# Performance work log

Measured on AMD Instinct MI355X. Metric: run time of the kernel, lower is better.

Reference implementation:

```python
import jax, jax.numpy as jnp
import numpy as np

N, E, DIN, H, DOUT, NBLK = 50000, 300000, 963, 256, 3, 6


def gconv(x, src, dst, ew, W, Wl, b):
    # support = x @ W ; out[i] = sum_j ew_ij * support[j] + x[i] @ W_loop + b
    sup = x @ W
    agg = jax.ops.segment_sum(ew[:, None] * sup[src], dst, num_segments=N)
    return agg + x @ Wl + b


def setup_inputs() -> dict:
    key = jax.random.key(0)
    ks = jax.random.split(key, 16)
    s = 0.05
    x = jax.random.normal(ks[0], (N, DIN), jnp.float32)
    src = jax.random.randint(ks[1], (E,), 0, N, dtype=jnp.int32)
    dst = jax.random.randint(ks[2], (E,), 0, N, dtype=jnp.int32)
    ew = jax.random.uniform(ks[3], (E,), jnp.float32)
    W1 = jax.random.normal(ks[4], (DIN, H), jnp.float32) * s
    Wl1 = jax.random.normal(ks[5], (DIN, H), jnp.float32) * s
    b1 = jnp.zeros((H,), jnp.float32)
    # stacked residual-block weights: [NBLK, 2 convs, H, H]
    blkW = jax.random.normal(ks[6], (NBLK, 2, H, H), jnp.float32) * s
    blkWl = jax.random.normal(ks[7], (NBLK, 2, H, H), jnp.float32) * s
    blkb = jnp.zeros((NBLK, 2, H), jnp.float32)
    W2 = jax.random.normal(ks[8], (H, DOUT), jnp.float32) * s
    Wl2 = jax.random.normal(ks[9], (H, DOUT), jnp.float32) * s
    b2 = jnp.zeros((DOUT,), jnp.float32)
    return dict(x=x, src=src, dst=dst, ew=ew, W1=W1, Wl1=Wl1, b1=b1,
                blkW=blkW, blkWl=blkWl, blkb=blkb, W2=W2, Wl2=Wl2, b2=b2)


def reference(x, src, dst, ew, W1, Wl1, b1, blkW, blkWl, blkb, W2, Wl2, b2):
    h = jax.nn.relu(gconv(x, src, dst, ew, W1, Wl1, b1))

    def block(h, p):
        W, Wl, b = p  # W: [2,H,H]
        y = jax.nn.relu(gconv(h, src, dst, ew, W[0], Wl[0], b[0]))
        y = jax.nn.relu(gconv(y, src, dst, ew, W[1], Wl[1], b[1]))
        return (h + y) * 0.5, None

    x_hidden, _ = jax.lax.scan(block, h, (blkW, blkWl, blkb))
    x_out = gconv(x_hidden, src, dst, ew, W2, Wl2, b2)
    return (x_out, x_hidden)
```

## Files before the change

kernel.cpp:

```cpp
#include <hip/hip_runtime.h>

typedef __attribute__((ext_vector_type(8))) short short8;
typedef __attribute__((ext_vector_type(4))) float f32x4;
typedef __attribute__((ext_vector_type(4), aligned(4))) float f32x4u;

constexpr int kN = 50000;
constexpr int kE = 300000;
constexpr int kDIN = 963;
constexpr int kH = 256;
constexpr int kNBLK = 6;

__device__ inline unsigned short f2bf(float f) {
    unsigned u = __float_as_uint(f);
    u = u + 0x7FFFu + ((u >> 16) & 1u);
    return (unsigned short)(u >> 16);
}
__device__ inline float bf2f(unsigned short s) {
    return __uint_as_float(((unsigned)s) << 16);
}

__device__ inline void gload_lds16(const void* g, void* l) {
    __builtin_amdgcn_global_load_lds(
        (const __attribute__((address_space(1))) void*)g,
        (__attribute__((address_space(3))) void*)l, 16, 0, 0);
}

__global__ __launch_bounds__(512) void gemm_l1(
    const float* __restrict__ Av, const unsigned short* __restrict__ Bt,
    const float* __restrict__ bias,
    unsigned short* __restrict__ supb, unsigned short* __restrict__ tpreb,
    int M, int Kpad, int Kvalid, int Astride)
{
    __shared__ __align__(16) char smem[81920];
    char* As  = smem;
    char* Bs0 = smem + 16384;
    char* Bs1 = smem + 49152;

    const int tid = threadIdx.x;
    const int wid = tid >> 6;
    const int lane = tid & 63;
    const int wr = wid >> 2, wc = wid & 3;

    const int nwg = gridDim.x;
    const int q = nwg >> 3, r = nwg & 7;
    const int xcd = blockIdx.x & 7, idx = blockIdx.x >> 3;
    const int t = (xcd < r ? xcd * (q + 1) : r * (q + 1) + (xcd - r) * q) + idx;
    const int r0 = t * 128;

    f32x4 acc[2][4][4];
#pragma unroll
    for (int hf = 0; hf < 2; ++hf)
#pragma unroll
        for (int i = 0; i < 4; ++i)
#pragma unroll
            for (int j = 0; j < 4; ++j) acc[hf][i][j] = f32x4{0.f, 0.f, 0.f, 0.f};

    const int l_row = lane >> 3;
    const int l_c   = lane & 7;

    for (int k0 = 0; k0 < Kpad; k0 += 64) {
#pragma unroll
        for (int p = 0; p < 4; ++p) {
            int row = wid * 32 + p * 8 + l_row;
            int csw = l_c ^ (row & 7);
            const unsigned short* g0 = Bt + (long)row * Kpad + k0 + csw * 8;
            gload_lds16(g0, Bs0 + (wid * 32 + p * 8) * 128);
            const unsigned short* g1 = Bt + (long)(256 + row) * Kpad + k0 + csw * 8;
            gload_lds16(g1, Bs1 + (wid * 32 + p * 8) * 128);
        }
        {
            const int row = tid >> 2;
            const int kq = tid & 3;
            int grow = r0 + row; if (grow >= M) grow = M - 1;
            const float* ar = Av + (long)grow * Astride;
#pragma unroll
            for (int j = 0; j < 2; ++j) {
                int k16 = kq * 2 + j;
                int kb = k0 + k16 * 8;
                short8 v;
                if (kb + 8 <= Kvalid) {
                    f32x4u f0 = *(const f32x4u*)(ar + kb);
                    f32x4u f1 = *(const f32x4u*)(ar + kb + 4);
#pragma unroll
                    for (int ii = 0; ii < 4; ++ii) {
                        v[ii]     = (short)f2bf(f0[ii]);
                        v[ii + 4] = (short)f2bf(f1[ii]);
                    }
                } else {
#pragma unroll
                    for (int ii = 0; ii < 8; ++ii) {
                        int k = kb + ii;
                        float f = (k < Kvalid) ? ar[k] : 0.f;
                        v[ii] = (short)f2bf(f);
                    }
                }
                *(short8*)(As + row * 128 + ((k16 ^ (row & 7)) << 4)) = v;
            }
        }
        __syncthreads();
#pragma unroll
        for (int kk = 0; kk < 2; ++kk) {
            const int kg = kk * 4 + (lane >> 4);
            short8 af[4];
#pragma unroll
            for (int nr = 0; nr < 4; ++nr) {
                int row = wr * 64 + nr * 16 + (lane & 15);
                af[nr] = *(const short8*)(As + row * 128 + ((kg ^ (row & 7)) << 4));
            }
#pragma unroll
            for (int hf = 0; hf < 2; ++hf) {
                const char* Bs = hf ? Bs1 : Bs0;
                short8 bfr[4];
#pragma unroll
                for (int mc = 0; mc < 4; ++mc) {
                    int row = wc * 64 + mc * 16 + (lane & 15);
                    bfr[mc] = *(const short8*)(Bs + row * 128 + ((kg ^ (row & 7)) << 4));
                }
#pragma unroll
                for (int mc = 0; mc < 4; ++mc)
#pragma unroll
                    for (int nr = 0; nr < 4; ++nr)
                        acc[hf][mc][nr] = __builtin_amdgcn_mfma_f32_16x16x32_bf16(
                            bfr[mc], af[nr], acc[hf][mc][nr], 0, 0, 0);
            }
        }
        __syncthreads();
    }

    float* eL = (float*)smem;
    const int wrow = wr * 16 + (lane & 15);
    const int qc = (lane >> 4) << 2;

#pragma unroll
    for (int hf = 0; hf < 2; ++hf) {
        unsigned short* outp = hf ? tpreb : supb;
        for (int nr = 0; nr < 4; ++nr) {
            __syncthreads();
#pragma unroll
            for (int mc = 0; mc < 4; ++mc) {
                const int col = wc * 64 + mc * 16 + qc;
                f32x4 v = acc[hf][mc][nr];
                if (hf) v += *(const f32x4*)(bias + col);
                const int c16 = col >> 2;
                *(f32x4*)(eL + wrow * 256 + ((c16 ^ wrow) << 2)) = v;
            }
            __syncthreads();
            const int tr = tid >> 4, j = tid & 15;
            const int gr = r0 + (tr >> 4) * 64 + nr * 16 + (tr & 15);
            if (gr < M) {
#pragma unroll
                for (int p = 0; p < 2; ++p) {
                    const int u = j + 16 * p;
                    f32x4 lo = *(const f32x4*)(eL + tr * 256 + (((2 * u) ^ tr) << 2));
                    f32x4 hi = *(const f32x4*)(eL + tr * 256 + (((2 * u + 1) ^ tr) << 2));
                    uint4 pk;
                    pk.x = (unsigned)f2bf(lo[0]) | ((unsigned)f2bf(lo[1]) << 16);
                    pk.y = (unsigned)f2bf(lo[2]) | ((unsigned)f2bf(lo[3]) << 16);
                    pk.z = (unsigned)f2bf(hi[0]) | ((unsigned)f2bf(hi[1]) << 16);
                    pk.w = (unsigned)f2bf(hi[2]) | ((unsigned)f2bf(hi[3]) << 16);
                    *(uint4*)(outp + (long)gr * 256 + u * 8) = pk;
                }
            }
        }
    }
}

template<int RES>
__global__ __launch_bounds__(256) void gemm_blk(
    const unsigned short* __restrict__ act, const unsigned short* __restrict__ xagg,
    const unsigned short* __restrict__ Bt, const float* __restrict__ bias,
    const unsigned short* __restrict__ hbf_res,
    unsigned short* __restrict__ outbf, float* __restrict__ hf32)
{
    __shared__ __align__(16) char smem[32768];
    char* As = smem;
    char* Bs = smem + 16384;

    const int tid = threadIdx.x;
    const int wid = tid >> 6;
    const int lane = tid & 63;
    const int wr = wid >> 1, wc = wid & 1;

    const int nwg = gridDim.x;
    const int q = nwg >> 3, r = nwg & 7;
    const int xcd = blockIdx.x & 7, idx = blockIdx.x >> 3;
    const int t = (xcd < r ? xcd * (q + 1) : r * (q + 1) + (xcd - r) * q) + idx;
    const int r0 = (t >> 1) * 128;
    const int c0 = (t & 1) * 128;

    f32x4 acc[4][4];
#pragma unroll
    for (int i = 0; i < 4; ++i)
#pragma unroll
        for (int j = 0; j < 4; ++j) acc[i][j] = f32x4{0.f, 0.f, 0.f, 0.f};

    const int l_row = lane >> 3;
    const int l_c   = lane & 7;

    for (int k0 = 0; k0 < 512; k0 += 64) {
#pragma unroll
        for (int p = 0; p < 4; ++p) {
            int row = wid * 32 + p * 8 + l_row;
            int csw = l_c ^ (row & 7);
            const unsigned short* g = Bt + (long)(c0 + row) * 512 + k0 + csw * 8;
            gload_lds16(g, Bs + (wid * 32 + p * 8) * 128);
        }
        const unsigned short* Asrc = (k0 < 256) ? (act + k0) : (xagg + (k0 - 256));
#pragma unroll
        for (int p = 0; p < 4; ++p) {
            int row = wid * 32 + p * 8 + l_row;
            int grow = r0 + row; if (grow >= kN) grow = kN - 1;
            int csw = l_c ^ (row & 7);
            const unsigned short* g = Asrc + (long)grow * 256 + csw * 8;
            gload_lds16(g, As + (wid * 32 + p * 8) * 128);
        }
        __syncthreads();
#pragma unroll
        for (int kk = 0; kk < 2; ++kk) {
            short8 af[4], bfr[4];
            const int kg = kk * 4 + (lane >> 4);
#pragma unroll
            for (int nr = 0; nr < 4; ++nr) {
                int row = wr * 64 + nr * 16 + (lane & 15);
                af[nr] = *(const short8*)(As + row * 128 + ((kg ^ (row & 7)) << 4));
            }
#pragma unroll
            for (int mc = 0; mc < 4; ++mc) {
                int row = wc * 64 + mc * 16 + (lane & 15);
                bfr[mc] = *(const short8*)(Bs + row * 128 + ((kg ^ (row & 7)) << 4));
            }
#pragma unroll
            for (int mc = 0; mc < 4; ++mc)
#pragma unroll
                for (int nr = 0; nr < 4; ++nr)
                    acc[mc][nr] = __builtin_amdgcn_mfma_f32_16x16x32_bf16(
                        bfr[mc], af[nr], acc[mc][nr], 0, 0, 0);
        }
        __syncthreads();
    }

    float* eL = (float*)smem;
    const int wrow = wr * 16 + (lane & 15);
    const int qc = (lane >> 4) << 2;

    for (int nr = 0; nr < 4; ++nr) {
        __syncthreads();
#pragma unroll
        for (int mc = 0; mc < 4; ++mc) {
            const int col = wc * 64 + mc * 16 + qc;
            f32x4 v = acc[mc][nr] + *(const f32x4*)(bias + c0 + col);
            const int c16 = col >> 2;
            *(f32x4*)(eL + wrow * 128 + ((c16 ^ wrow) << 2)) = v;
        }
        __syncthreads();
        const int tr = tid >> 3, j = tid & 7;
        const int gr = r0 + (tr >> 4) * 64 + nr * 16 + (tr & 15);
        if (gr < kN) {
#pragma unroll
            for (int p = 0; p < 2; ++p) {
                const int u = j + 8 * p;
                f32x4 lo = *(const f32x4*)(eL + tr * 128 + (((2 * u) ^ tr) << 2));
                f32x4 hi = *(const f32x4*)(eL + tr * 128 + (((2 * u + 1) ^ tr) << 2));
#pragma unroll
                for (int ii = 0; ii < 4; ++ii) {
                    lo[ii] = fmaxf(lo[ii], 0.f);
                    hi[ii] = fmaxf(hi[ii], 0.f);
                }
                const long gcol = (long)gr * 256 + c0 + u * 8;
                if (RES >= 1) {
                    uint4 hv = *(const uint4*)(hbf_res + gcol);
                    lo[0] = (bf2f((unsigned short)(hv.x & 0xFFFF)) + lo[0]) * 0.5f;
                    lo[1] = (bf2f((unsigned short)(hv.x >> 16))    + lo[1]) * 0.5f;
                    lo[2] = (bf2f((unsigned short)(hv.y & 0xFFFF)) + lo[2]) * 0.5f;
                    lo[3] = (bf2f((unsigned short)(hv.y >> 16))    + lo[3]) * 0.5f;
                    hi[0] = (bf2f((unsigned short)(hv.z & 0xFFFF)) + hi[0]) * 0.5f;
                    hi[1] = (bf2f((unsigned short)(hv.z >> 16))    + hi[1]) * 0.5f;
                    hi[2] = (bf2f((unsigned short)(hv.w & 0xFFFF)) + hi[2]) * 0.5f;
                    hi[3] = (bf2f((unsigned short)(hv.w >> 16))    + hi[3]) * 0.5f;
                }
                if (RES == 2) {
                    *(f32x4*)(hf32 + gcol)     = lo;
                    *(f32x4*)(hf32 + gcol + 4) = hi;
                }
                uint4 pk;
                pk.x = (unsigned)f2bf(lo[0]) | ((unsigned)f2bf(lo[1]) << 16);
                pk.y = (unsigned)f2bf(lo[2]) | ((unsigned)f2bf(lo[3]) << 16);
                pk.z = (unsigned)f2bf(hi[0]) | ((unsigned)f2bf(hi[1]) << 16);
                pk.w = (unsigned)f2bf(hi[2]) | ((unsigned)f2bf(hi[3]) << 16);
                *(uint4*)(outbf + gcol) = pk;
            }
        }
    }
}

template<int MODE>
__global__ __launch_bounds__(256) void agg16_kernel(
    const unsigned short* __restrict__ srcbuf, const unsigned short* __restrict__ tpreb,
    const int* __restrict__ rowptr, const int* __restrict__ e_src,
    const float* __restrict__ e_w, unsigned short* __restrict__ outb)
{
    const int tid = threadIdx.x;
    const int sub = tid >> 5;
    const int l   = tid & 31;
    const long node = (long)blockIdx.x * 8 + sub;
    if (node >= kN) return;
    const int c0 = l * 8;

    f32x4 a0 = {0.f, 0.f, 0.f, 0.f}, a1 = {0.f, 0.f, 0.f, 0.f};
    if (MODE == 1) {
        uint4 tv = *(const uint4*)(tpreb + node * 256 + c0);
        a0[0] = bf2f((unsigned short)(tv.x & 0xFFFF)); a0[1] = bf2f((unsigned short)(tv.x >> 16));
        a0[2] = bf2f((unsigned short)(tv.y & 0xFFFF)); a0[3] = bf2f((unsigned short)(tv.y >> 16));
        a1[0] = bf2f((unsigned short)(tv.z & 0xFFFF)); a1[1] = bf2f((unsigned short)(tv.z >> 16));
        a1[2] = bf2f((unsigned short)(tv.w & 0xFFFF)); a1[3] = bf2f((unsigned short)(tv.w >> 16));
    }

    int b = rowptr[node];
    const int e = rowptr[node + 1];

#define ACC16(V, W) \
    a0[0] += (W) * bf2f((unsigned short)((V).x & 0xFFFF)); \
    a0[1] += (W) * bf2f((unsigned short)((V).x >> 16));    \
    a0[2] += (W) * bf2f((unsigned short)((V).y & 0xFFFF)); \
    a0[3] += (W) * bf2f((unsigned short)((V).y >> 16));    \
    a1[0] += (W) * bf2f((unsigned short)((V).z & 0xFFFF)); \
    a1[1] += (W) * bf2f((unsigned short)((V).z >> 16));    \
    a1[2] += (W) * bf2f((unsigned short)((V).w & 0xFFFF)); \
    a1[3] += (W) * bf2f((unsigned short)((V).w >> 16));

    for (; b + 4 <= e; b += 4) {
        const int s0 = e_src[b],     s1 = e_src[b + 1];
        const int s2 = e_src[b + 2], s3 = e_src[b + 3];
        const float w0 = e_w[b],     w1 = e_w[b + 1];
        const float w2 = e_w[b + 2], w3 = e_w[b + 3];
        uint4 v0 = *(const uint4*)(srcbuf + (long)s0 * 256 + c0);
        uint4 v1 = *(const uint4*)(srcbuf + (long)s1 * 256 + c0);
        uint4 v2 = *(const uint4*)(srcbuf + (long)s2 * 256 + c0);
        uint4 v3 = *(const uint4*)(srcbuf + (long)s3 * 256 + c0);
        ACC16(v0, w0) ACC16(v1, w1) ACC16(v2, w2) ACC16(v3, w3)
    }
    for (; b < e; ++b) {
        const int s = e_src[b];
        const float w = e_w[b];
        uint4 v = *(const uint4*)(srcbuf + (long)s * 256 + c0);
        ACC16(v, w)
    }
#undef ACC16

    if (MODE == 1) {
#pragma unroll
        for (int ii = 0; ii < 4; ++ii) {
            a0[ii] = fmaxf(a0[ii], 0.f);
            a1[ii] = fmaxf(a1[ii], 0.f);
        }
    }
    uint4 pk;
    pk.x = (unsigned)f2bf(a0[0]) | ((unsigned)f2bf(a0[1]) << 16);
    pk.y = (unsigned)f2bf(a0[2]) | ((unsigned)f2bf(a0[3]) << 16);
    pk.z = (unsigned)f2bf(a1[0]) | ((unsigned)f2bf(a1[1]) << 16);
    pk.w = (unsigned)f2bf(a1[2]) | ((unsigned)f2bf(a1[3]) << 16);
    *(uint4*)(outb + node * 256 + c0) = pk;
}

__global__ __launch_bounds__(256) void cvt_w1_kernel(
    const float* __restrict__ W1, const float* __restrict__ Wl1,
    unsigned short* __restrict__ out)
{
    int idx = blockIdx.x * 256 + threadIdx.x;
    if (idx >= 512 * 1024) return;
    int c = idx >> 10, k = idx & 1023;
    float v = 0.f;
    if (k < kDIN) v = (c < 256) ? W1[(long)k * 256 + c] : Wl1[(long)k * 256 + (c - 256)];
    out[idx] = f2bf(v);
}

__global__ __launch_bounds__(256) void cvt_blk_kernel(
    const float* __restrict__ blkW, const float* __restrict__ blkWl,
    unsigned short* __restrict__ out)
{
    int idx = blockIdx.x * 256 + threadIdx.x;
    if (idx >= 12 * 256 * 512) return;
    int l = idx >> 17;
    int rem = idx & 131071;
    int c = rem >> 9, k = rem & 511;
    float v = (k < 256) ? blkWl[((long)l * 256 + k) * 256 + c]
                        : blkW[((long)l * 256 + (k - 256)) * 256 + c];
    out[idx] = f2bf(v);
}

__global__ __launch_bounds__(256) void hist_kernel(const int* __restrict__ dst,
                                                   int* __restrict__ counts)
{
    int e = blockIdx.x * 256 + threadIdx.x;
    if (e < kE) atomicAdd(&counts[dst[e]], 1);
}

__global__ __launch_bounds__(1024) void scan1_kernel(
    const int* __restrict__ counts, int* __restrict__ rowptr, int* __restrict__ bsum)
{
    __shared__ int s[1024];
    const int tid = threadIdx.x;
    const int g = blockIdx.x * 1024 + tid;
    const int v = (g < kN) ? counts[g] : 0;
    s[tid] = v; __syncthreads();
    for (int off = 1; off < 1024; off <<= 1) {
        int tv = (tid >= off) ? s[tid - off] : 0;
        __syncthreads();
        s[tid] += tv;
        __syncthreads();
    }
    if (g < kN) rowptr[g] = s[tid] - v;
    if (tid == 1023) bsum[blockIdx.x] = s[1023];
}

__global__ __launch_bounds__(64) void scan2_kernel(int* __restrict__ bsum, int nb)
{
    __shared__ int s[64];
    const int tid = threadIdx.x;
    const int v = (tid < nb) ? bsum[tid] : 0;
    s[tid] = v; __syncthreads();
    for (int off = 1; off < 64; off <<= 1) {
        int tv = (tid >= off) ? s[tid - off] : 0;
        __syncthreads();
        s[tid] += tv;
        __syncthreads();
    }
    if (tid < nb) bsum[tid] = s[tid] - v;
}

__global__ __launch_bounds__(256) void scan3_kernel(
    int* __restrict__ rowptr, const int* __restrict__ bsum, int* __restrict__ cursor)
{
    int g = blockIdx.x * 256 + threadIdx.x;
    if (g < kN) {
        int r = rowptr[g] + bsum[g >> 10];
        rowptr[g] = r;
        cursor[g] = r;
    }
    if (g == 0) rowptr[kN] = kE;
}

__global__ __launch_bounds__(256) void fill_kernel(
    const int* __restrict__ src, const int* __restrict__ dst,
    const float* __restrict__ ew, int* __restrict__ cursor,
    int* __restrict__ e_src, float* __restrict__ e_w)
{
    int e = blockIdx.x * 256 + threadIdx.x;
    if (e >= kE) return;
    int d = dst[e];
    int pos = atomicAdd(&cursor[d], 1);
    e_src[pos] = src[e];
    e_w[pos] = ew[e];
}

__global__ __launch_bounds__(64) void final_layer_kernel(
    const unsigned short* __restrict__ hbf, const float* __restrict__ W2,
    const float* __restrict__ Wl2, const float* __restrict__ b2,
    float* __restrict__ sup2, float* __restrict__ x_out)
{
    const int row = blockIdx.x;
    const int lane = threadIdx.x;
    const unsigned short* hr = hbf + (long)row * kH;
    float accW[3] = {0.f, 0.f, 0.f};
    float accL[3] = {0.f, 0.f, 0.f};
#pragma unroll
    for (int kb = 0; kb < kH / 64; ++kb) {
        int k = kb * 64 + lane;
        float v = bf2f(hr[k]);
#pragma unroll
        for (int c = 0; c < 3; ++c) {
            accW[c] = fmaf(v, W2[k * 3 + c], accW[c]);
            accL[c] = fmaf(v, Wl2[k * 3 + c], accL[c]);
        }
    }
#pragma unroll
    for (int off = 32; off > 0; off >>= 1) {
#pragma unroll
        for (int c = 0; c < 3; ++c) {
            accW[c] += __shfl_down(accW[c], off);
            accL[c] += __shfl_down(accL[c], off);
        }
    }
    if (lane == 0) {
#pragma unroll
        for (int c = 0; c < 3; ++c) {
            sup2[row * 3 + c] = accW[c];
            x_out[row * 3 + c] = accL[c] + b2[c];
        }
    }
}

__global__ __launch_bounds__(256) void scatter3_kernel(
    const float* __restrict__ sup2, const int* __restrict__ src,
    const int* __restrict__ dst, const float* __restrict__ ew,
    float* __restrict__ x_out)
{
    int e = blockIdx.x * 256 + threadIdx.x;
    if (e >= kE) return;
    int s = src[e];
    int d = dst[e];
    float w = ew[e];
#pragma unroll
    for (int c = 0; c < 3; ++c)
        atomicAdd(&x_out[(long)d * 3 + c], w * sup2[(long)s * 3 + c]);
}

extern "C" void kernel_launch(void* const* d_in, const int* in_sizes, int n_in,
                              void* d_out, int out_size, void* d_ws, size_t ws_size,
                              hipStream_t stream)
{
    const float* x    = (const float*)d_in[0];
    const int*   src  = (const int*)d_in[1];
    const int*   dst  = (const int*)d_in[2];
    const float* ew   = (const float*)d_in[3];
    const float* W1   = (const float*)d_in[4];
    const float* Wl1  = (const float*)d_in[5];
    const float* b1   = (const float*)d_in[6];
    const float* blkW  = (const float*)d_in[7];
    const float* blkWl = (const float*)d_in[8];
    const float* blkb  = (const float*)d_in[9];
    const float* W2   = (const float*)d_in[10];
    const float* Wl2  = (const float*)d_in[11];
    const float* b2   = (const float*)d_in[12];

    float* out   = (float*)d_out;
    float* x_out = out;
    float* h     = out + (long)kN * 3;

    char* w = (char*)d_ws;
    size_t off = 0;
    auto carve = [&](size_t bytes) { char* p = w + off; off = (off + bytes + 255) & ~(size_t)255; return p; };
    unsigned short* supb  = (unsigned short*)carve(12800000UL * 2);
    unsigned short* tpreb = (unsigned short*)carve(12800000UL * 2);
    unsigned short* tact  = (unsigned short*)carve(12800000UL * 2);
    unsigned short* hbf   = (unsigned short*)carve(12800000UL * 2);
    unsigned short* w1c   = (unsigned short*)carve(512UL * 1024 * 2);
    unsigned short* blkc  = (unsigned short*)carve(12UL * 256 * 512 * 2);
    int*   e_src  = (int*)carve(kE * 4);
    float* e_w    = (float*)carve(kE * 4);
    int*   counts = (int*)carve(50176 * 4);
    int*   rowptr = (int*)carve(50176 * 4);
    int*   cursor = (int*)carve(50176 * 4);
    int*   bsum   = (int*)carve(64 * 4);
    float* sup2   = (float*)carve((long)kN * 3 * 4);
    unsigned short* xagg = tpreb;

    hipMemsetAsync(counts, 0, 50176 * 4, stream);
    hist_kernel<<<(kE + 255) / 256, 256, 0, stream>>>(dst, counts);
    scan1_kernel<<<49, 1024, 0, stream>>>(counts, rowptr, bsum);
    scan2_kernel<<<1, 64, 0, stream>>>(bsum, 49);
    scan3_kernel<<<(kN + 255) / 256, 256, 0, stream>>>(rowptr, bsum, cursor);
    fill_kernel<<<(kE + 255) / 256, 256, 0, stream>>>(src, dst, ew, cursor, e_src, e_w);

    cvt_w1_kernel<<<2048, 256, 0, stream>>>(W1, Wl1, w1c);
    cvt_blk_kernel<<<6144, 256, 0, stream>>>(blkW, blkWl, blkc);

    const int l1_grid  = (kN + 127) / 128;
    const int blk_grid = 2 * ((kN + 127) / 128);
    const int agg_grid = (kN + 7) / 8;

    gemm_l1<<<l1_grid, 512, 0, stream>>>(x, w1c, b1, supb, tpreb,
                                         kN, 1024, kDIN, kDIN);
    agg16_kernel<1><<<agg_grid, 256, 0, stream>>>(supb, tpreb, rowptr, e_src, e_w, hbf);

    for (int l = 0; l < 2 * kNBLK; ++l) {
        const unsigned short* act_in = (l & 1) ? tact : hbf;
        unsigned short* act_out      = (l & 1) ? hbf : tact;
        agg16_kernel<0><<<agg_grid, 256, 0, stream>>>(act_in, nullptr, rowptr, e_src, e_w, xagg);
        const unsigned short* B = blkc + (long)l * 256 * 512;
        const float* bb = blkb + (long)l * 256;
        if (l & 1) {
            if (l == 2 * kNBLK - 1)
                gemm_blk<2><<<blk_grid, 256, 0, stream>>>(act_in, xagg, B, bb, hbf, act_out, h);
            else
                gemm_blk<1><<<blk_grid, 256, 0, stream>>>(act_in, xagg, B, bb, hbf, act_out, nullptr);
        } else {
            gemm_blk<0><<<blk_grid, 256, 0, stream>>>(act_in, xagg, B, bb, nullptr, act_out, nullptr);
        }
    }

    final_layer_kernel<<<kN, 64, 0, stream>>>(hbf, W2, Wl2, b2, sup2, x_out);
    scatter3_kernel<<<(kE + 255) / 256, 256, 0, stream>>>(sup2, src, dst, ew, x_out);
}
```

Before: 955.1 us.

## Pre-convert x to padded bf16 and split layer-1 GEMM by output half; widen aggregation per lane

Adds a pass that converts x to a zero-padded bf16 buffer, then runs a new layer-1 GEMM that streams A and B straight into LDS with async global-to-LDS loads. The grid is split so each workgroup computes either the support or the self-loop half, using an XCD-aware tile mapping. This avoids converting fp32 to bf16 inside the GEMM mainloop, at the cost of an extra ~100MB write and read pass and of reading the A tile twice. The aggregation kernel now uses 16 lanes per node with 32-byte loads per lane, doubling the work per lane and halving the number of threads.

```diff
diff --git a/kernel.cpp b/kernel.cpp
--- a/kernel.cpp
+++ b/kernel.cpp
@@ -23,6 +23,138 @@
     __builtin_amdgcn_global_load_lds(
         (const __attribute__((address_space(1))) void*)g,
         (__attribute__((address_space(3))) void*)l, 16, 0, 0);
+}
+
+__global__ __launch_bounds__(128) void xcvt_kernel(
+    const float* __restrict__ x, unsigned short* __restrict__ xbf)
+{
+    const int row = blockIdx.x;
+    const int kb = threadIdx.x * 8;
+    const float* xr = x + (long)row * kDIN;
+    short8 v;
+    if (kb + 8 <= kDIN) {
+        f32x4u f0 = *(const f32x4u*)(xr + kb);
+        f32x4u f1 = *(const f32x4u*)(xr + kb + 4);
+#pragma unroll
+        for (int ii = 0; ii < 4; ++ii) {
+            v[ii]     = (short)f2bf(f0[ii]);
+            v[ii + 4] = (short)f2bf(f1[ii]);
+        }
+    } else {
+#pragma unroll
+        for (int ii = 0; ii < 8; ++ii) {
+            int k = kb + ii;
+            v[ii] = (short)((k < kDIN) ? f2bf(xr[k]) : 0);
+        }
+    }
+    *(short8*)(xbf + (long)row * 1024 + kb) = v;
+}
+
+__global__ __launch_bounds__(512) void gemm_l1_bf(
+    const unsigned short* __restrict__ xbf, const unsigned short* __restrict__ Bt,
+    const float* __restrict__ bias,
+    unsigned short* __restrict__ supb, unsigned short* __restrict__ tpreb)
+{
+    __shared__ __align__(16) char smem[49152];
+    char* As = smem;
+    char* Bs = smem + 16384;
+
+    const int tid = threadIdx.x;
+    const int wid = tid >> 6;
+    const int lane = tid & 63;
+    const int wr = wid >> 2, wc = wid & 3;
+
+    const int nwg = gridDim.x;
+    const int q = nwg >> 3, r = nwg & 7;
+    const int xcd = blockIdx.x & 7, idx = blockIdx.x >> 3;
+    const int t = (xcd < r ? xcd * (q + 1) : r * (q + 1) + (xcd - r) * q) + idx;
+    const int r0 = (t >> 1) * 128;
+    const int c0 = (t & 1) * 256;
+
+    f32x4 acc[4][4];
+#pragma unroll
+    for (int i = 0; i < 4; ++i)
+#pragma unroll
+        for (int j = 0; j < 4; ++j) acc[i][j] = f32x4{0.f, 0.f, 0.f, 0.f};
+
+    const int l_row = lane >> 3;
+    const int l_c   = lane & 7;
+
+    for (int k0 = 0; k0 < 1024; k0 += 64) {
+#pragma unroll
+        for (int p = 0; p < 4; ++p) {
+            int row = wid * 32 + p * 8 + l_row;
+            int csw = l_c ^ (row & 7);
+            const unsigned short* g = Bt + (long)(c0 + row) * 1024 + k0 + csw * 8;
+            gload_lds16(g, Bs + (wid * 32 + p * 8) * 128);
+        }
+#pragma unroll
+        for (int p = 0; p < 2; ++p) {
+            int row = wid * 16 + p * 8 + l_row;
+            int grow = r0 + row; if (grow >= kN) grow = kN - 1;
+            int csw = l_c ^ (row & 7);
+            const unsigned short* g = xbf + (long)grow * 1024 + k0 + csw * 8;
+            gload_lds16(g, As + (wid * 16 + p * 8) * 128);
+        }
+        __syncthreads();
+#pragma unroll
+        for (int kk = 0; kk < 2; ++kk) {
+            short8 af[4], bfr[4];
+            const int kg = kk * 4 + (lane >> 4);
+#pragma unroll
+            for (int nr = 0; nr < 4; ++nr) {
+                int row = wr * 64 + nr * 16 + (lane & 15);
+                af[nr] = *(const short8*)(As + row * 128 + ((kg ^ (row & 7)) << 4));
+            }
+#pragma unroll
+            for (int mc = 0; mc < 4; ++mc) {
+                int row = wc * 64 + mc * 16 + (lane & 15);
+                bfr[mc] = *(const short8*)(Bs + row * 128 + ((kg ^ (row & 7)) << 4));
+            }
+#pragma unroll
+            for (int mc = 0; mc < 4; ++mc)
+#pragma unroll
+                for (int nr = 0; nr < 4; ++nr)
+                    acc[mc][nr] = __builtin_amdgcn_mfma_f32_16x16x32_bf16(
+                        bfr[mc], af[nr], acc[mc][nr], 0, 0, 0);
+        }
+        __syncthreads();
+    }
+
+    const bool isSup = (c0 == 0);
+    unsigned short* outp = isSup ? supb : tpreb;
+    float* eL = (float*)smem;
+    const int wrow = wr * 16 + (lane & 15);
+    const int qc = (lane >> 4) << 2;
+
+    for (int nr = 0; nr < 4; ++nr) {
+        __syncthreads();
+#pragma unroll
+        for (int mc = 0; mc < 4; ++mc) {
+            const int col = wc * 64 + mc * 16 + qc;
+            f32x4 v = acc[mc][nr];
+            if (!isSup) v += *(const f32x4*)(bias + col);
+            const int c16 = col >> 2;
+            *(f32x4*)(eL + wrow * 256 + ((c16 ^ wrow) << 2)) = v;
+        }
+        __syncthreads();
+        const int tr = tid >> 4, j = tid & 15;
+        const int gr = r0 + (tr >> 4) * 64 + nr * 16 + (tr & 15);
+        if (gr < kN) {
+#pragma unroll
+            for (int p = 0; p < 2; ++p) {
+                const int u = j + 16 * p;
+                f32x4 lo = *(const f32x4*)(eL + tr * 256 + (((2 * u) ^ tr) << 2));
+                f32x4 hi = *(const f32x4*)(eL + tr * 256 + (((2 * u + 1) ^ tr) << 2));
+                uint4 pk;
+                pk.x = (unsigned)f2bf(lo[0]) | ((unsigned)f2bf(lo[1]) << 16);
+                pk.y = (unsigned)f2bf(lo[2]) | ((unsigned)f2bf(lo[3]) << 16);
+                pk.z = (unsigned)f2bf(hi[0]) | ((unsigned)f2bf(hi[1]) << 16);
+                pk.w = (unsigned)f2bf(hi[2]) | ((unsigned)f2bf(hi[3]) << 16);
+                *(uint4*)(outp + (long)gr * 256 + u * 8) = pk;
+            }
+        }
+    }
 }
 
 __global__ __launch_bounds__(512) void gemm_l1(
@@ -147,7 +279,7 @@
             __syncthreads();
             const int tr = tid >> 4, j = tid & 15;
             const int gr = r0 + (tr >> 4) * 64 + nr * 16 + (tr & 15);
-            if (gr < M) {
+            if (gr < kN) {
 #pragma unroll
                 for (int p = 0; p < 2; ++p) {
                     const int u = j + 16 * p;
@@ -300,66 +432,81 @@
     const float* __restrict__ e_w, unsigned short* __restrict__ outb)
 {
     const int tid = threadIdx.x;
-    const int sub = tid >> 5;
-    const int l   = tid & 31;
-    const long node = (long)blockIdx.x * 8 + sub;
+    const int sub = tid >> 4;
+    const int l   = tid & 15;
+    const long node = (long)blockIdx.x * 16 + sub;
     if (node >= kN) return;
-    const int c0 = l * 8;
-
-    f32x4 a0 = {0.f, 0.f, 0.f, 0.f}, a1 = {0.f, 0.f, 0.f, 0.f};
+    const int c0 = l * 16;
+
+    f32x4 a0 = {0.f,0.f,0.f,0.f}, a1 = {0.f,0.f,0.f,0.f};
+    f32x4 a2 = {0.f,0.f,0.f,0.f}, a3 = {0.f,0.f,0.f,0.f};
+
+#define UNPK(A0, A1, V, W) \
+    A0[0] += (W) * bf2f((unsigned short)((V).x & 0xFFFF)); \
+    A0[1] += (W) * bf2f((unsigned short)((V).x >> 16));    \
+    A0[2] += (W) * bf2f((unsigned short)((V).y & 0xFFFF)); \
+    A0[3] += (W) * bf2f((unsigned short)((V).y >> 16));    \
+    A1[0] += (W) * bf2f((unsigned short)((V).z & 0xFFFF)); \
+    A1[1] += (W) * bf2f((unsigned short)((V).z >> 16));    \
+    A1[2] += (W) * bf2f((unsigned short)((V).w & 0xFFFF)); \
+    A1[3] += (W) * bf2f((unsigned short)((V).w >> 16));
+
     if (MODE == 1) {
-        uint4 tv = *(const uint4*)(tpreb + node * 256 + c0);
-        a0[0] = bf2f((unsigned short)(tv.x & 0xFFFF)); a0[1] = bf2f((unsigned short)(tv.x >> 16));
-        a0[2] = bf2f((unsigned short)(tv.y & 0xFFFF)); a0[3] = bf2f((unsigned short)(tv.y >> 16));
-        a1[0] = bf2f((unsigned short)(tv.z & 0xFFFF)); a1[1] = bf2f((unsigned short)(tv.z >> 16));
-        a1[2] = bf2f((unsigned short)(tv.w & 0xFFFF)); a1[3] = bf2f((unsigned short)(tv.w >> 16));
+        uint4 t0 = *(const uint4*)(tpreb + node * 256 + c0);
+        uint4 t1 = *(const uint4*)(tpreb + node * 256 + c0 + 8);
+        UNPK(a0, a1, t0, 1.f)
+        UNPK(a2, a3, t1, 1.f)
     }
 
     int b = rowptr[node];
     const int e = rowptr[node + 1];
-
-#define ACC16(V, W) \
-    a0[0] += (W) * bf2f((unsigned short)((V).x & 0xFFFF)); \
-    a0[1] += (W) * bf2f((unsigned short)((V).x >> 16));    \
-    a0[2] += (W) * bf2f((unsigned short)((V).y & 0xFFFF)); \
-    a0[3] += (W) * bf2f((unsigned short)((V).y >> 16));    \
-    a1[0] += (W) * bf2f((unsigned short)((V).z & 0xFFFF)); \
-    a1[1] += (W) * bf2f((unsigned short)((V).z >> 16));    \
-    a1[2] += (W) * bf2f((unsigned short)((V).w & 0xFFFF)); \
-    a1[3] += (W) * bf2f((unsigned short)((V).w >> 16));
 
     for (; b + 4 <= e; b += 4) {
         const int s0 = e_src[b],     s1 = e_src[b + 1];
         const int s2 = e_src[b + 2], s3 = e_src[b + 3];
         const float w0 = e_w[b],     w1 = e_w[b + 1];
         const float w2 = e_w[b + 2], w3 = e_w[b + 3];
-        uint4 v0 = *(const uint4*)(srcbuf + (long)s0 * 256 + c0);
-        uint4 v1 = *(const uint4*)(srcbuf + (long)s1 * 256 + c0);
-        uint4 v2 = *(const uint4*)(srcbuf + (long)s2 * 256 + c0);
-        uint4 v3 = *(const uint4*)(srcbuf + (long)s3 * 256 + c0);
-        ACC16(v0, w0) ACC16(v1, w1) ACC16(v2, w2) ACC16(v3, w3)
+        const unsigned short* p0 = srcbuf + (long)s0 * 256 + c0;
+        const unsigned short* p1 = srcbuf + (long)s1 * 256 + c0;
+        const unsigned short* p2 = srcbuf + (long)s2 * 256 + c0;
+        const unsigned short* p3 = srcbuf + (long)s3 * 256 + c0;
+        uint4 va0 = *(const uint4*)(p0),     vb0 = *(const uint4*)(p0 + 8);
+        uint4 va1 = *(const uint4*)(p1),     vb1 = *(const uint4*)(p1 + 8);
+        uint4 va2 = *(const uint4*)(p2),     vb2 = *(const uint4*)(p2 + 8);
+        uint4 va3 = *(const uint4*)(p3),     vb3 = *(const uint4*)(p3 + 8);
+        UNPK(a0, a1, va0, w0) UNPK(a2, a3, vb0, w0)
+        UNPK(a0, a1, va1, w1) UNPK(a2, a3, vb1, w1)
+        UNPK(a0, a1, va2, w2) UNPK(a2, a3, vb2, w2)
+        UNPK(a0, a1, va3, w3) UNPK(a2, a3, vb3, w3)
     }
     for (; b < e; ++b) {
         const int s = e_src[b];
         const float w = e_w[b];
-        uint4 v = *(const uint4*)(srcbuf + (long)s * 256 + c0);
-        ACC16(v, w)
-    }
-#undef ACC16
+        const unsigned short* p = srcbuf + (long)s * 256 + c0;
+        uint4 va = *(const uint4*)(p);
+        uint4 vb = *(const uint4*)(p + 8);
+        UNPK(a0, a1, va, w) UNPK(a2, a3, vb, w)
+    }
+#undef UNPK
 
     if (MODE == 1) {
 #pragma unroll
         for (int ii = 0; ii < 4; ++ii) {
-            a0[ii] = fmaxf(a0[ii], 0.f);
-            a1[ii] = fmaxf(a1[ii], 0.f);
-        }
-    }
-    uint4 pk;
-    pk.x = (unsigned)f2bf(a0[0]) | ((unsigned)f2bf(a0[1]) << 16);
-    pk.y = (unsigned)f2bf(a0[2]) | ((unsigned)f2bf(a0[3]) << 16);
-    pk.z = (unsigned)f2bf(a1[0]) | ((unsigned)f2bf(a1[1]) << 16);
-    pk.w = (unsigned)f2bf(a1[2]) | ((unsigned)f2bf(a1[3]) << 16);
-    *(uint4*)(outb + node * 256 + c0) = pk;
+            a0[ii] = fmaxf(a0[ii], 0.f); a1[ii] = fmaxf(a1[ii], 0.f);
+            a2[ii] = fmaxf(a2[ii], 0.f); a3[ii] = fmaxf(a3[ii], 0.f);
+        }
+    }
+    uint4 pk0, pk1;
+    pk0.x = (unsigned)f2bf(a0[0]) | ((unsigned)f2bf(a0[1]) << 16);
+    pk0.y = (unsigned)f2bf(a0[2]) | ((unsigned)f2bf(a0[3]) << 16);
+    pk0.z = (unsigned)f2bf(a1[0]) | ((unsigned)f2bf(a1[1]) << 16);
+    pk0.w = (unsigned)f2bf(a1[2]) | ((unsigned)f2bf(a1[3]) << 16);
+    pk1.x = (unsigned)f2bf(a2[0]) | ((unsigned)f2bf(a2[1]) << 16);
+    pk1.y = (unsigned)f2bf(a2[2]) | ((unsigned)f2bf(a2[3]) << 16);
+    pk1.z = (unsigned)f2bf(a3[0]) | ((unsigned)f2bf(a3[1]) << 16);
+    pk1.w = (unsigned)f2bf(a3[2]) | ((unsigned)f2bf(a3[3]) << 16);
+    *(uint4*)(outb + node * 256 + c0)     = pk0;
+    *(uint4*)(outb + node * 256 + c0 + 8) = pk1;
 }
 
 __global__ __launch_bounds__(256) void cvt_w1_kernel(
@@ -545,6 +692,11 @@
     float* sup2   = (float*)carve((long)kN * 3 * 4);
     unsigned short* xagg = tpreb;
 
+    const size_t xbf_bytes = (size_t)kN * 1024 * 2;
+    unsigned short* xbf = nullptr;
+    if (off + xbf_bytes + 256 <= ws_size)
+        xbf = (unsigned short*)carve(xbf_bytes);
+
     hipMemsetAsync(counts, 0, 50176 * 4, stream);
     hist_kernel<<<(kE + 255) / 256, 256, 0, stream>>>(dst, counts);
     scan1_kernel<<<49, 1024, 0, stream>>>(counts, rowptr, bsum);
@@ -555,12 +707,17 @@
     cvt_w1_kernel<<<2048, 256, 0, stream>>>(W1, Wl1, w1c);
     cvt_blk_kernel<<<6144, 256, 0, stream>>>(blkW, blkWl, blkc);
 
-    const int l1_grid  = (kN + 127) / 128;
+    const int l1_grid  = 2 * ((kN + 127) / 128);
     const int blk_grid = 2 * ((kN + 127) / 128);
-    const int agg_grid = (kN + 7) / 8;
-
-    gemm_l1<<<l1_grid, 512, 0, stream>>>(x, w1c, b1, supb, tpreb,
-                                         kN, 1024, kDIN, kDIN);
+    const int agg_grid = (kN + 15) / 16;
+
+    if (xbf) {
+        xcvt_kernel<<<kN, 128, 0, stream>>>(x, xbf);
+        gemm_l1_bf<<<l1_grid, 512, 0, stream>>>(xbf, w1c, b1, supb, tpreb);
+    } else {
+        gemm_l1<<<(kN + 127) / 128, 512, 0, stream>>>(x, w1c, b1, supb, tpreb,
+                                                      kN, 1024, kDIN, kDIN);
+    }
     agg16_kernel<1><<<agg_grid, 256, 0, stream>>>(supb, tpreb, rowptr, e_src, e_w, hbf);
 
     for (int l = 0; l < 2 * kNBLK; ++l) {
```

After: 1.030 ms. +7.9%, slower.
